# Kernel optimization log

Hardware: AMD Instinct MI355X
Metric: run time of the kernel (lower is better)

Reference implementation:

```python
import jax, jax.numpy as jnp
import numpy as np

# Config constants from the module
E = 64    # n_routed_experts
K = 6     # num_experts_per_tok
D = 128   # hidden_size
M = 80    # moe_intermediate_size
MS = 160  # shared expert intermediate = moe_intermediate_size * n_shared_experts
B, S = 64, 256

def _init_w(k, shape, fan_in):
    # kaiming_uniform(a=sqrt(5)) used by nn.Linear / MoEGate: bound = 1/sqrt(fan_in)
    bound = 1.0 / np.sqrt(fan_in)
    return jax.random.uniform(k, shape, jnp.float32, -bound, bound)

def setup_inputs() -> dict:
    key = jax.random.key(0)
    ks = jax.random.split(key, 8)
    return {
        "hidden_states": jax.random.normal(ks[0], (B, S, D), jnp.float32),
        "gate_w": _init_w(ks[1], (E, D), D),        # MoEGate.linear.weight [E, gating_dim]
        "wg": _init_w(ks[2], (E, D, M), D),          # stacked expert gate_proj (transposed)
        "wu": _init_w(ks[3], (E, D, M), D),          # stacked expert up_proj
        "wd": _init_w(ks[4], (E, M, D), M),          # stacked expert down_proj
        "swg": _init_w(ks[5], (D, MS), D),           # shared expert gate_proj
        "swu": _init_w(ks[6], (D, MS), D),           # shared expert up_proj
        "swd": _init_w(ks[7], (MS, D), MS),          # shared expert down_proj
    }

def reference(hidden_states, gate_w, wg, wu, wd, swg, swu, swd):
    orig_shape = hidden_states.shape
    x = hidden_states.reshape(-1, D)                       # [T, D] flat tokens
    T = x.shape[0]
    # --- MoEGate ('all_agent' mode): softmax scoring + top-k + renorm ---
    scores = jax.nn.softmax(x @ gate_w.T, axis=-1)          # [T, E]
    topk_w, topk_idx = jax.lax.top_k(scores, K)             # [T, K]
    topk_w = topk_w / (jnp.sum(topk_w, axis=-1, keepdims=True) + 1e-20)
    # Scatter top-k weights into dense per-expert combine weights [T, E]
    cw = jnp.zeros_like(scores).at[jnp.arange(T)[:, None], topk_idx].add(topk_w)
    # --- Routed experts: SiLU-gated MLP per expert, combined by cw ---
    g = jax.nn.silu(jnp.einsum('td,edm->tem', x, wg)) * jnp.einsum('td,edm->tem', x, wu)
    y = jnp.einsum('tem,emd,te->td', g, wd, cw)             # down-proj + weighted combine
    # --- Shared experts ---
    shared = (jax.nn.silu(x @ swg) * (x @ swu)) @ swd       # [T, D]
    return (y + shared).reshape(orig_shape)
```

## Files before the change

kernel.cpp:

```cpp
#include <hip/hip_runtime.h>
#include <hip/hip_bf16.h>
#include <math.h>


typedef unsigned short ushort_t;
typedef __attribute__((ext_vector_type(8))) short bf16x8;
typedef __attribute__((ext_vector_type(4))) float f32x4;

#define EALL  66

#define OFF_TOPKI 16384
#define OFF_WORK  409600
#define OFF_TOPKW 802816
#define OFF_PERM  1196032
#define OFF_PERMW 1589248
#define OFF_POS2  1982464
#define OFF_YPERM 2375680
#define OFF_YSH   27541504
#define OFF_WGT   31735808
#define OFF_WUT   33087488
#define OFF_WDP   34439168
#define OFF_XB    36061184
#define OFF_HIST  40255488
#define OFF_BOFF  40321024
#define NEED_FAST 40386560
#define FOFF_YBUF 2375680
#define FOFF_WGT  10764288
#define FOFF_WUT  12115968
#define FOFF_WDP  13467648
#define FOFF_XB   15089664
#define FOFF_HIST 19283968
#define FOFF_BOFF 19349504

__device__ __forceinline__ float bf2f(ushort_t u) {
    unsigned int x = ((unsigned int)u) << 16;
    float f; __builtin_memcpy(&f, &x, 4); return f;
}
__device__ __forceinline__ ushort_t f2bf(float f) {
    unsigned int x; __builtin_memcpy(&x, &f, 4);
    unsigned int r = (x + 0x7fffu + ((x >> 16) & 1u)) >> 16;
    return (ushort_t)r;
}
__device__ __forceinline__ float ldin(const void* p, int i, int f32m) {
    return f32m ? ((const float*)p)[i] : bf2f(((const ushort_t*)p)[i]);
}
__device__ __forceinline__ int detect_f32m(const ushort_t* gw) {
    int lane = threadIdx.x & 63;
    int cnt = 0;
    #pragma unroll
    for (int j = 0; j < 4; ++j) {
        ushort_t u = gw[lane * 4 + j];
        if (((u >> 7) & 0xFF) >= 0x7C) cnt++;
    }
    #pragma unroll
    for (int off = 32; off; off >>= 1) cnt += __shfl_xor(cnt, off);
    return (cnt >= 8) ? 1 : 0;
}
__device__ __forceinline__ void gl16(void* l, const void* g) {
    __builtin_amdgcn_global_load_lds(
        (const __attribute__((address_space(1))) void*)g,
        (__attribute__((address_space(3))) void*)l, 16, 0, 0);
}

__global__ __launch_bounds__(1024) void k_pg(const void* x, const void* gw,
        const void* wg, const void* wu, const void* wd,
        const void* swg, const void* swu, const void* swd,
        ushort_t* wgT, ushort_t* wuT, ushort_t* wdP,
        ushort_t* xB, int* topk_i, float* topk_w, int* histPart) {
    __shared__ __align__(16) char smem[41984];
    int tid = threadIdx.x, bid = blockIdx.x;
    int f32m = detect_f32m((const ushort_t*)gw);

    if (bid < 3 * EALL) {
        float* lds = (float*)smem;
        int mat = bid / EALL, e = bid % EALL;
        if (mat < 2) {
            const void* src  = (mat == 0) ? wg  : wu;
            const void* ssrc = (mat == 0) ? swg : swu;
            for (int i = tid; i < 10240; i += 1024) {
                int d = i / 80, m = i % 80;
                float v = (e < 64) ? ldin(src, e * 10240 + i, f32m)
                                   : ldin(ssrc, d * 160 + (e - 64) * 80 + m, f32m);
                lds[d * 81 + m] = v;
            }
            __syncthreads();
            ushort_t* dst = ((mat == 0) ? wgT : wuT) + e * 10240;
            for (int o = tid; o < 10240; o += 1024) {
                int m = o >> 7, d = o & 127;
                dst[o] = f2bf(lds[d * 81 + m]);
            }
        } else {
            for (int i = tid; i < 10240; i += 1024) {
                float v = (e < 64) ? ldin(wd, e * 10240 + i, f32m)
                                   : ldin(swd, (e - 64) * 10240 + i, f32m);
                int m = i >> 7, d = i & 127;
                lds[m * 129 + d] = v;
            }
            __syncthreads();
            ushort_t* dst = wdP + e * 12288;
            for (int o = tid; o < 12288; o += 1024) {
                int d = o / 96, m = o % 96;
                dst[o] = (m < 80) ? f2bf(lds[m * 129 + d]) : (ushort_t)0;
            }
        }
        return;
    }

    float* gwl  = (float*)smem;
    float (*xl)[128] = (float(*)[128])(smem + 33280);
    int*   histL = (int*)(smem + 41472);
    int b = bid - 3 * EALL;
    for (int i = tid; i < 8192; i += 1024)
        gwl[(i >> 7) * 130 + (i & 127)] = ldin(gw, i, f32m);
    if (tid < 64) histL[tid] = 0;
    __syncthreads();
    int wv = tid >> 6, lane = tid & 63;
    for (int q = 0; q < 4; ++q) {
        int t = b * 64 + wv * 4 + q;
        float xv0, xv1;
        if (f32m) {
            float2 v = ((const float2*)((const float*)x + t * 128))[lane];
            xv0 = v.x; xv1 = v.y;
        } else {
            unsigned int pr = *(const unsigned int*)((const ushort_t*)x + t * 128 + lane * 2);
            xv0 = bf2f((ushort_t)(pr & 0xffffu));
            xv1 = bf2f((ushort_t)(pr >> 16));
        }
        float2 xw; xw.x = xv0; xw.y = xv1;
        *(float2*)&xl[wv][lane * 2] = xw;
        unsigned int packed = (unsigned int)f2bf(xv0) | ((unsigned int)f2bf(xv1) << 16);
        *(unsigned int*)(xB + t * 128 + lane * 2) = packed;
        float acc = 0.f;
        #pragma unroll
        for (int d2 = 0; d2 < 64; ++d2) {
            float2 xv = *(const float2*)&xl[wv][d2 * 2];
            float2 gv = *(const float2*)&gwl[lane * 130 + d2 * 2];
            acc = fmaf(xv.x, gv.x, acc);
            acc = fmaf(xv.y, gv.y, acc);
        }
        float mx = acc;
        #pragma unroll
        for (int off = 32; off; off >>= 1) mx = fmaxf(mx, __shfl_xor(mx, off));
        float p = expf(acc - mx);
        float sm = p;
        #pragma unroll
        for (int off = 32; off; off >>= 1) sm += __shfl_xor(sm, off);
        float sc = p / sm;
        float cur = sc;
        float wk6[6]; int ik[6];
        #pragma unroll
        for (int k = 0; k < 6; ++k) {
            float bv = cur; int bi = lane;
            #pragma unroll
            for (int off = 1; off < 64; off <<= 1) {
                float ov = __shfl_xor(bv, off); int oi = __shfl_xor(bi, off);
                if (ov > bv || (ov == bv && oi < bi)) { bv = ov; bi = oi; }
            }
            wk6[k] = bv; ik[k] = bi;
            if (lane == bi) cur = -INFINITY;
        }
        if (lane == 0) {
            float den = wk6[0] + wk6[1] + wk6[2] + wk6[3] + wk6[4] + wk6[5] + 1e-20f;
            #pragma unroll
            for (int k = 0; k < 6; ++k) {
                topk_i[t * 6 + k] = ik[k];
                topk_w[t * 6 + k] = wk6[k] / den;
                atomicAdd(&histL[ik[k]], 1);
            }
        }
    }
    __syncthreads();
    if (tid < 64) histPart[tid * 256 + b] = histL[tid];
}

__global__ __launch_bounds__(256) void k_scatter(int* Wi, const int* histPart,
        const int* topk_i, const float* topk_w, int* perm, float* permw, int* pos2) {
    __shared__ int hl[16384];
    __shared__ int cntL[64], exclL[64], lcur[64];
    int tid = threadIdx.x, lane = tid & 63, wv = tid >> 6, b = blockIdx.x;
    for (int j = tid; j < 16384; j += 256) hl[j] = histPart[j];
    __syncthreads();
    for (int ei = 0; ei < 16; ++ei) {
        int e = wv * 16 + ei;
        int carry = 0;
        for (int r = 0; r < 4; ++r) {
            int v = hl[e * 256 + r * 64 + lane];
            int incl = v;
            #pragma unroll
            for (int off = 1; off < 64; off <<= 1) {
                int ts = __shfl_up(incl, off);
                if (lane >= off) incl += ts;
            }
            hl[e * 256 + r * 64 + lane] = carry + incl - v;
            carry += __shfl(incl, 63);
        }
        if (lane == 0) cntL[e] = carry;
    }
    __syncthreads();
    if (tid == 0) {
        int s = 0;
        for (int e = 0; e < 64; ++e) { exclL[e] = s; s += cntL[e]; }
    }
    __syncthreads();
    if (b == 0 && tid < 64) { Wi[tid] = cntL[tid]; Wi[64 + tid] = exclL[tid]; }
    if (tid < 64) lcur[tid] = hl[tid * 256 + b] + exclL[tid];
    __syncthreads();
    for (int i = tid; i < 384; i += 256) {
        int g = b * 384 + i;
        int e = topk_i[g];
        float w = topk_w[g];
        int p = atomicAdd(&lcur[e], 1);
        perm[p]  = b * 64 + i / 6;
        permw[p] = w;
        pos2[g]  = p;
    }
}

template<int FAST>
__global__ __launch_bounds__(256) void k_expert(const ushort_t* x, const ushort_t* wgT,
        const ushort_t* wuT, const ushort_t* wdP, const int* Wi,
        const int* perm, const float* permw, ushort_t* yperm, ushort_t* ysh, float* ybuf) {
    __shared__ __align__(16) char hl[32768];
    __shared__ __align__(16) char bufA[8192];
    __shared__ __align__(16) char bufB[8192];

    int tid = threadIdx.x, lid = tid & 63, wv = tid >> 6;
    int bid = blockIdx.x;
    int kg  = (lid >> 4) * 16;
    int kq8 = (lid >> 4) * 8;

    int e, c;
    if (bid < 256) {
        e = 64; c = bid;
    } else {
        int cnt_l = Wi[lid];
        int nc = (cnt_l + 127) >> 7;
        int incl = nc;
        #pragma unroll
        for (int off = 1; off < 64; off <<= 1) {
            int t2 = __shfl_up(incl, off);
            if (lid >= off) incl += t2;
        }
        int totalR = __shfl(incl, 63);
        int rb = bid - 256;
        if (rb >= totalR) return;
        int epref = incl - nc;
        unsigned long long m = __ballot(rb >= epref && rb < incl);
        int src = (int)__builtin_ctzll(m);
        e = src;
        c = rb - __shfl(epref, src);
    }

    if (e < 64) {
        int n = Wi[e], base = Wi[64 + e];
        int nrows = n - c * 128; if (nrows > 128) nrows = 128;

        bf16x8 a[2][4];
        #pragma unroll
        for (int tr = 0; tr < 2; ++tr) {
            int arow = wv * 32 + tr * 16 + (lid & 15);
            int r = (arow < nrows) ? arow : (nrows - 1);
            int t = perm[base + c * 128 + r];
            #pragma unroll
            for (int k = 0; k < 4; ++k)
                a[tr][k] = *(const bf16x8*)(x + t * 128 + k * 32 + kq8);
        }

        const ushort_t* gS = wgT + e * 10240;
        const ushort_t* uS = wuT + e * 10240;

        #pragma unroll
        for (int g = 0; g < 3; ++g) {
            int rbase = g * 32;
            int units = (g == 2) ? 256 : 512;
            #pragma unroll
            for (int i = 0; i < 2; ++i) {
                int s = i * 256 + tid;
                if (s < units) {
                    int row = rbase + (s >> 4);
                    int sc = (s & 15) ^ (row & 7);
                    gl16(bufA + (size_t)s * 16, gS + row * 128 + sc * 8);
                    gl16(bufB + (size_t)s * 16, uS + row * 128 + sc * 8);
                }
            }
            __syncthreads();
            int nmi = (g == 2) ? 1 : 2;
            for (int m2 = 0; m2 < nmi; ++m2) {
                int mi = 2 * g + m2;
                int brow = mi * 16 + (lid & 15);
                int lro = (brow - rbase) * 256;
                int bsw = (brow & 7) << 4;
                f32x4 ag[2], au[2];
                #pragma unroll
                for (int tr = 0; tr < 2; ++tr) {
                    ag[tr] = (f32x4){0.f, 0.f, 0.f, 0.f};
                    au[tr] = (f32x4){0.f, 0.f, 0.f, 0.f};
                }
                #pragma unroll
                for (int k = 0; k < 4; ++k) {
                    int bo = lro + (((k * 64) + kg) ^ bsw);
                    bf16x8 bg = *(const bf16x8*)(bufA + bo);
                    bf16x8 bu = *(const bf16x8*)(bufB + bo);
                    #pragma unroll
                    for (int tr = 0; tr < 2; ++tr) {
                        ag[tr] = __builtin_amdgcn_mfma_f32_16x16x32_bf16(a[tr][k], bg, ag[tr], 0, 0, 0);
                        au[tr] = __builtin_amdgcn_mfma_f32_16x16x32_bf16(a[tr][k], bu, au[tr], 0, 0, 0);
                    }
                }
                #pragma unroll
                for (int tr = 0; tr < 2; ++tr) {
                    #pragma unroll
                    for (int rg = 0; rg < 4; ++rg) {
                        float gg = ag[tr][rg], uu2 = au[tr][rg];
                        float h = (gg / (1.f + __expf(-gg))) * uu2;
                        int row = wv * 32 + tr * 16 + (lid >> 4) * 4 + rg;
                        int cb = (mi * 16 + (lid & 15)) * 2;
                        *(ushort_t*)(hl + row * 256 + (cb ^ ((row & 7) << 4))) = f2bf(h);
                    }
                }
            }
            __syncthreads();
        }

        {
            int r = wv * 32 + (lid >> 1), ch = 10 + (lid & 1);
            uint4 z = {0u, 0u, 0u, 0u};
            *(uint4*)(hl + r * 256 + ((ch * 16) ^ ((r & 7) << 4))) = z;
        }
        bf16x8 bfr[2][3];
        #pragma unroll
        for (int tf = 0; tf < 2; ++tf) {
            int brow = wv * 32 + tf * 16 + (lid & 15);
            #pragma unroll
            for (int k = 0; k < 3; ++k)
                bfr[tf][k] = *(const bf16x8*)(hl + brow * 256 + (((k * 64) + kg) ^ ((brow & 7) << 4)));
        }

        f32x4 acc[8][2];
        #pragma unroll
        for (int dt = 0; dt < 8; ++dt) {
            acc[dt][0] = (f32x4){0.f, 0.f, 0.f, 0.f};
            acc[dt][1] = (f32x4){0.f, 0.f, 0.f, 0.f};
        }
        const ushort_t* dS = wdP + e * 12288;
        #pragma unroll
        for (int h = 0; h < 2; ++h) {
            #pragma unroll
            for (int i = 0; i < 2; ++i) {
                int s = i * 256 + tid;
                int r = s >> 4, ch = s & 15;
                int rowA = h * 64 + r;
                int scA = ch ^ (rowA & 7);
                int offA = (scA < 12) ? scA * 8 : 0;
                gl16(bufA + (size_t)s * 16, dS + rowA * 96 + offA);
                int rowB = rowA + 32;
                int scB = ch ^ (rowB & 7);
                int offB = (scB < 12) ? scB * 8 : 0;
                gl16(bufB + (size_t)s * 16, dS + rowB * 96 + offB);
            }
            __syncthreads();
            #pragma unroll
            for (int d2 = 0; d2 < 4; ++d2) {
                int dt = h * 4 + d2;
                int grow = dt * 16 + (lid & 15);
                int lr = (d2 & 1) * 16 + (lid & 15);
                const char* wb = (d2 < 2) ? bufA : bufB;
                bf16x8 ad[3];
                #pragma unroll
                for (int k = 0; k < 3; ++k)
                    ad[k] = *(const bf16x8*)(wb + lr * 256 + (((k * 64) + kg) ^ ((grow & 7) << 4)));
                #pragma unroll
                for (int tf = 0; tf < 2; ++tf) {
                    f32x4 cc = acc[dt][tf];
                    #pragma unroll
                    for (int k = 0; k < 3; ++k)
                        cc = __builtin_amdgcn_mfma_f32_16x16x32_bf16(ad[k], bfr[tf][k], cc, 0, 0, 0);
                    acc[dt][tf] = cc;
                }
            }
            __syncthreads();
        }

        #pragma unroll
        for (int tf = 0; tf < 2; ++tf) {
            int rloc = wv * 32 + tf * 16 + (lid & 15);
            int rc = (rloc < nrows) ? rloc : (nrows - 1);
            float w = FAST ? permw[base + c * 128 + rc] : 0.f;
            #pragma unroll
            for (int dt = 0; dt < 8; ++dt) {
                if (FAST) {
                    int cb = (dt * 16 + (lid >> 4) * 4) * 2;
                    ushort_t o[4];
                    #pragma unroll
                    for (int rg = 0; rg < 4; ++rg) o[rg] = f2bf(acc[dt][tf][rg] * w);
                    *(uint2*)(hl + rloc * 256 + (cb ^ ((rloc & 7) << 4))) = *(const uint2*)o;
                } else {
                    if (rloc < nrows) {
                        int t = perm[base + c * 128 + rloc];
                        float w2 = permw[base + c * 128 + rloc];
                        int d0 = dt * 16 + (lid >> 4) * 4;
                        #pragma unroll
                        for (int rg = 0; rg < 4; ++rg)
                            atomicAdd(&ybuf[t * 128 + d0 + rg], acc[dt][tf][rg] * w2);
                    }
                }
            }
        }
        if (FAST) {
            #pragma unroll
            for (int ps = 0; ps < 8; ++ps) {
                int row = wv * 32 + ps * 4 + (lid >> 4);
                int cb = (lid & 15) * 16;
                uint4 v = *(const uint4*)(hl + row * 256 + (cb ^ ((row & 7) << 4)));
                if (row < nrows)
                    *(uint4*)(yperm + (size_t)(base + c * 128 + row) * 128 + (lid & 15) * 8) = v;
            }
        }
    } else {
        bf16x8 a1[4];
        int arow = wv * 16 + (lid & 15);
        int t0 = c * 64 + arow;
        #pragma unroll
        for (int k = 0; k < 4; ++k)
            a1[k] = *(const bf16x8*)(x + t0 * 128 + k * 32 + kq8);

        f32x4 acc[8];
        #pragma unroll
        for (int dt = 0; dt < 8; ++dt) acc[dt] = (f32x4){0.f, 0.f, 0.f, 0.f};

        for (int sub = 0; sub < 2; ++sub) {
            int ee = 64 + sub;
            const ushort_t* gS = wgT + ee * 10240;
            const ushort_t* uS = wuT + ee * 10240;

            #pragma unroll
            for (int g = 0; g < 3; ++g) {
                int rbase = g * 32;
                int units = (g == 2) ? 256 : 512;
                #pragma unroll
                for (int i = 0; i < 2; ++i) {
                    int s = i * 256 + tid;
                    if (s < units) {
                        int row = rbase + (s >> 4);
                        int sc = (s & 15) ^ (row & 7);
                        gl16(bufA + (size_t)s * 16, gS + row * 128 + sc * 8);
                        gl16(bufB + (size_t)s * 16, uS + row * 128 + sc * 8);
                    }
                }
                __syncthreads();
                int nmi = (g == 2) ? 1 : 2;
                for (int m2 = 0; m2 < nmi; ++m2) {
                    int mi = 2 * g + m2;
                    int brow = mi * 16 + (lid & 15);
                    int lro = (brow - rbase) * 256;
                    int bsw = (brow & 7) << 4;
                    f32x4 ag = {0.f, 0.f, 0.f, 0.f};
                    f32x4 au = {0.f, 0.f, 0.f, 0.f};
                    #pragma unroll
                    for (int k = 0; k < 4; ++k) {
                        int bo = lro + (((k * 64) + kg) ^ bsw);
                        bf16x8 bg = *(const bf16x8*)(bufA + bo);
                        bf16x8 bu = *(const bf16x8*)(bufB + bo);
                        ag = __builtin_amdgcn_mfma_f32_16x16x32_bf16(a1[k], bg, ag, 0, 0, 0);
                        au = __builtin_amdgcn_mfma_f32_16x16x32_bf16(a1[k], bu, au, 0, 0, 0);
                    }
                    #pragma unroll
                    for (int rg = 0; rg < 4; ++rg) {
                        float gg = ag[rg], uu2 = au[rg];
                        float h = (gg / (1.f + __expf(-gg))) * uu2;
                        int row = wv * 16 + (lid >> 4) * 4 + rg;
                        int cb = (mi * 16 + (lid & 15)) * 2;
                        *(ushort_t*)(hl + row * 256 + (cb ^ ((row & 7) << 4))) = f2bf(h);
                    }
                }
                __syncthreads();
            }
            if (sub == 0 && lid < 32) {
                int r = wv * 16 + (lid >> 1), ch = 10 + (lid & 1);
                uint4 z = {0u, 0u, 0u, 0u};
                *(uint4*)(hl + r * 256 + ((ch * 16) ^ ((r & 7) << 4))) = z;
            }
            bf16x8 bfr1[3];
            {
                int brow = wv * 16 + (lid & 15);
                #pragma unroll
                for (int k = 0; k < 3; ++k)
                    bfr1[k] = *(const bf16x8*)(hl + brow * 256 + (((k * 64) + kg) ^ ((brow & 7) << 4)));
            }

            const ushort_t* dS = wdP + ee * 12288;
            #pragma unroll
            for (int h = 0; h < 2; ++h) {
                #pragma unroll
                for (int i = 0; i < 2; ++i) {
                    int s = i * 256 + tid;
                    int r = s >> 4, ch = s & 15;
                    int rowA = h * 64 + r;
                    int scA = ch ^ (rowA & 7);
                    int offA = (scA < 12) ? scA * 8 : 0;
                    gl16(bufA + (size_t)s * 16, dS + rowA * 96 + offA);
                    int rowB = rowA + 32;
                    int scB = ch ^ (rowB & 7);
                    int offB = (scB < 12) ? scB * 8 : 0;
                    gl16(bufB + (size_t)s * 16, dS + rowB * 96 + offB);
                }
                __syncthreads();
                #pragma unroll
                for (int d2 = 0; d2 < 4; ++d2) {
                    int dt = h * 4 + d2;
                    int grow = dt * 16 + (lid & 15);
                    int lr = (d2 & 1) * 16 + (lid & 15);
                    const char* wb = (d2 < 2) ? bufA : bufB;
                    bf16x8 ad[3];
                    #pragma unroll
                    for (int k = 0; k < 3; ++k)
                        ad[k] = *(const bf16x8*)(wb + lr * 256 + (((k * 64) + kg) ^ ((grow & 7) << 4)));
                    f32x4 cc = acc[dt];
                    #pragma unroll
                    for (int k = 0; k < 3; ++k)
                        cc = __builtin_amdgcn_mfma_f32_16x16x32_bf16(ad[k], bfr1[k], cc, 0, 0, 0);
                    acc[dt] = cc;
                }
                __syncthreads();
            }
        }

        int rloc = wv * 16 + (lid & 15);
        if (FAST) {
            #pragma unroll
            for (int dt = 0; dt < 8; ++dt) {
                int cb = (dt * 16 + (lid >> 4) * 4) * 2;
                ushort_t o[4];
                #pragma unroll
                for (int rg = 0; rg < 4; ++rg) o[rg] = f2bf(acc[dt][rg]);
                *(uint2*)(hl + rloc * 256 + (cb ^ ((rloc & 7) << 4))) = *(const uint2*)o;
            }
            #pragma unroll
            for (int ps = 0; ps < 4; ++ps) {
                int row = wv * 16 + ps * 4 + (lid >> 4);
                int cb = (lid & 15) * 16;
                uint4 v = *(const uint4*)(hl + row * 256 + (cb ^ ((row & 7) << 4)));
                *(uint4*)(ysh + (size_t)(c * 64 + row) * 128 + (lid & 15) * 8) = v;
            }
        } else {
            int t = c * 64 + rloc;
            #pragma unroll
            for (int dt = 0; dt < 8; ++dt) {
                int d0 = dt * 16 + (lid >> 4) * 4;
                #pragma unroll
                for (int rg = 0; rg < 4; ++rg)
                    atomicAdd(&ybuf[t * 128 + d0 + rg], acc[dt][rg]);
            }
        }
    }
}

__global__ __launch_bounds__(256) void k_final_gather(const ushort_t* yperm,
        const ushort_t* ysh, const int* pos2, void* out, const ushort_t* gwDet) {
    int idx = blockIdx.x * 256 + threadIdx.x;
    int t = idx >> 4, cg = (idx & 15) * 8;
    int f32m = detect_f32m(gwDet);
    float acc[8];
    {
        uint4 v = *(const uint4*)(ysh + (size_t)t * 128 + cg);
        const ushort_t* u = (const ushort_t*)&v;
        #pragma unroll
        for (int j = 0; j < 8; ++j) acc[j] = bf2f(u[j]);
    }
    const int* pp = pos2 + t * 6;
    #pragma unroll
    for (int k = 0; k < 6; ++k) {
        int p = pp[k];
        uint4 v = *(const uint4*)(yperm + (size_t)p * 128 + cg);
        const ushort_t* u = (const ushort_t*)&v;
        #pragma unroll
        for (int j = 0; j < 8; ++j) acc[j] += bf2f(u[j]);
    }
    if (f32m) {
        float4 o0 = {acc[0], acc[1], acc[2], acc[3]};
        float4 o1 = {acc[4], acc[5], acc[6], acc[7]};
        float* op = (float*)out + (size_t)t * 128 + cg;
        *(float4*)op = o0; *(float4*)(op + 4) = o1;
    } else {
        ushort_t o[8];
        #pragma unroll
        for (int j = 0; j < 8; ++j) o[j] = f2bf(acc[j]);
        *(uint4*)((ushort_t*)out + (size_t)t * 128 + cg) = *(const uint4*)o;
    }
}

__global__ __launch_bounds__(256) void k_final_ybuf(const float* ybuf, void* out,
        const ushort_t* gwDet) {
    int i = blockIdx.x * 256 + threadIdx.x;
    int f32m = detect_f32m(gwDet);
    float4 v = ((const float4*)ybuf)[i];
    if (f32m) {
        ((float4*)out)[i] = v;
    } else {
        ushort4 o;
        o.x = f2bf(v.x); o.y = f2bf(v.y); o.z = f2bf(v.z); o.w = f2bf(v.w);
        ((ushort4*)out)[i] = o;
    }
}

extern "C" void kernel_launch(void* const* d_in, const int* in_sizes, int n_in,
                              void* d_out, int out_size, void* d_ws, size_t ws_size,
                              hipStream_t stream) {
    (void)in_sizes; (void)n_in; (void)out_size;
    const void* x   = d_in[0];
    const void* gw  = d_in[1];
    const void* wg  = d_in[2];
    const void* wu  = d_in[3];
    const void* wd  = d_in[4];
    const void* swg = d_in[5];
    const void* swu = d_in[6];
    const void* swd = d_in[7];

    char* ws = (char*)d_ws;
    int fast = (ws_size >= (size_t)NEED_FAST) ? 1 : 0;

    int*      Wi     = (int*)d_ws;
    int*      topk_i = (int*)(ws + OFF_TOPKI);
    float*    topk_w = (float*)(ws + OFF_TOPKW);
    int*      perm   = (int*)(ws + OFF_PERM);
    float*    permw  = (float*)(ws + OFF_PERMW);
    int*      pos2   = (int*)(ws + OFF_POS2);

    ushort_t* yperm = (ushort_t*)(ws + OFF_YPERM);
    ushort_t* ysh   = (ushort_t*)(ws + OFF_YSH);
    float*    ybuf  = (float*)(ws + FOFF_YBUF);
    ushort_t* wgT   = (ushort_t*)(ws + (fast ? OFF_WGT  : FOFF_WGT));
    ushort_t* wuT   = (ushort_t*)(ws + (fast ? OFF_WUT  : FOFF_WUT));
    ushort_t* wdP   = (ushort_t*)(ws + (fast ? OFF_WDP  : FOFF_WDP));
    ushort_t* xB    = (ushort_t*)(ws + (fast ? OFF_XB   : FOFF_XB));
    int*      histP = (int*)(ws + (fast ? OFF_HIST : FOFF_HIST));

    if (!fast) hipMemsetAsync(ybuf, 0, 16384 * 128 * 4, stream);

    k_pg<<<3 * EALL + 256, 1024, 0, stream>>>(x, gw, wg, wu, wd, swg, swu, swd,
                                              wgT, wuT, wdP, xB, topk_i, topk_w, histP);
    k_scatter<<<256, 256, 0, stream>>>(Wi, histP, topk_i, topk_w, perm, permw, pos2);
    if (fast) {
        k_expert<1><<<1088, 256, 0, stream>>>(xB, wgT, wuT, wdP, Wi, perm, permw, yperm, ysh, ybuf);
        k_final_gather<<<1024, 256, 0, stream>>>(yperm, ysh, pos2, d_out, (const ushort_t*)gw);
    } else {
        k_expert<0><<<1088, 256, 0, stream>>>(xB, wgT, wuT, wdP, Wi, perm, permw, yperm, ysh, ybuf);
        k_final_ybuf<<<2048, 256, 0, stream>>>(ybuf, d_out, (const ushort_t*)gw);
    }
}
```

Baseline: 93.53 us.

## Prefetch expert gate/up and down weights into larger LDS buffers upfront

Enlarges the LDS weight staging buffers so that most of the gate/up weights and the whole down-projection matrix are loaded asynchronously at the start of each expert block. The global-to-LDS transfers then overlap with the token gather and the gate/up MFMA work. This cuts the number of load/sync rounds from five to two per expert. The down-projection matrix gets a new 192-byte row layout with a split swizzle, which avoids the padded 256-byte rows and the dummy loads. LDS use per block rises to about 80KB, which may lower occupancy.

```diff
diff --git a/kernel.cpp b/kernel.cpp
--- a/kernel.cpp
+++ b/kernel.cpp
@@ -10,7 +10,6 @@
 #define EALL  66
 
 #define OFF_TOPKI 16384
-#define OFF_WORK  409600
 #define OFF_TOPKW 802816
 #define OFF_PERM  1196032
 #define OFF_PERMW 1589248
@@ -61,6 +60,9 @@
         (const __attribute__((address_space(1))) void*)g,
         (__attribute__((address_space(3))) void*)l, 16, 0, 0);
 }
+__device__ __forceinline__ int dswz(int ch, int r) {
+    return (ch < 8) ? (ch ^ (r & 7)) : (8 + ((ch - 8) ^ (r & 3)));
+}
 
 __global__ __launch_bounds__(1024) void k_pg(const void* x, const void* gw,
         const void* wg, const void* wu, const void* wd,
@@ -221,8 +223,8 @@
         const ushort_t* wuT, const ushort_t* wdP, const int* Wi,
         const int* perm, const float* permw, ushort_t* yperm, ushort_t* ysh, float* ybuf) {
     __shared__ __align__(16) char hl[32768];
-    __shared__ __align__(16) char bufA[8192];
-    __shared__ __align__(16) char bufB[8192];
+    __shared__ __align__(16) char bufW[24576];
+    __shared__ __align__(16) char bufD[24576];
 
     int tid = threadIdx.x, lid = tid & 63, wv = tid >> 6;
     int bid = blockIdx.x;
@@ -255,6 +257,26 @@
         int n = Wi[e], base = Wi[64 + e];
         int nrows = n - c * 128; if (nrows > 128) nrows = 128;
 
+        const ushort_t* gS = wgT + e * 10240;
+        const ushort_t* uS = wuT + e * 10240;
+        const ushort_t* dS = wdP + e * 12288;
+
+        #pragma unroll
+        for (int i = 0; i < 3; ++i) {
+            int u = i * 256 + tid;
+            int r = u >> 4, ch = u & 15;
+            int cc = ch ^ (r & 7);
+            gl16(bufW + (size_t)u * 16, gS + r * 128 + cc * 8);
+            gl16(bufW + 12288 + (size_t)u * 16, uS + r * 128 + cc * 8);
+        }
+        #pragma unroll
+        for (int i = 0; i < 6; ++i) {
+            int u = i * 256 + tid;
+            int r = u / 12, d = u % 12;
+            int cc = dswz(d, r);
+            gl16(bufD + (size_t)u * 16, dS + r * 96 + cc * 8);
+        }
+
         bf16x8 a[2][4];
         #pragma unroll
         for (int tr = 0; tr < 2; ++tr) {
@@ -265,61 +287,86 @@
             for (int k = 0; k < 4; ++k)
                 a[tr][k] = *(const bf16x8*)(x + t * 128 + k * 32 + kq8);
         }
-
-        const ushort_t* gS = wgT + e * 10240;
-        const ushort_t* uS = wuT + e * 10240;
-
-        #pragma unroll
-        for (int g = 0; g < 3; ++g) {
-            int rbase = g * 32;
-            int units = (g == 2) ? 256 : 512;
-            #pragma unroll
-            for (int i = 0; i < 2; ++i) {
-                int s = i * 256 + tid;
-                if (s < units) {
-                    int row = rbase + (s >> 4);
-                    int sc = (s & 15) ^ (row & 7);
-                    gl16(bufA + (size_t)s * 16, gS + row * 128 + sc * 8);
-                    gl16(bufB + (size_t)s * 16, uS + row * 128 + sc * 8);
-                }
-            }
-            __syncthreads();
-            int nmi = (g == 2) ? 1 : 2;
-            for (int m2 = 0; m2 < nmi; ++m2) {
-                int mi = 2 * g + m2;
-                int brow = mi * 16 + (lid & 15);
-                int lro = (brow - rbase) * 256;
-                int bsw = (brow & 7) << 4;
-                f32x4 ag[2], au[2];
+        __syncthreads();
+
+        #pragma unroll
+        for (int mi = 0; mi < 3; ++mi) {
+            int brow = mi * 16 + (lid & 15);
+            int bro = brow * 256, bsw = (brow & 7) << 4;
+            f32x4 ag[2], au[2];
+            #pragma unroll
+            for (int tr = 0; tr < 2; ++tr) {
+                ag[tr] = (f32x4){0.f, 0.f, 0.f, 0.f};
+                au[tr] = (f32x4){0.f, 0.f, 0.f, 0.f};
+            }
+            #pragma unroll
+            for (int k = 0; k < 4; ++k) {
+                int bo = bro + (((k * 64) + kg) ^ bsw);
+                bf16x8 bg = *(const bf16x8*)(bufW + bo);
+                bf16x8 bu = *(const bf16x8*)(bufW + 12288 + bo);
                 #pragma unroll
                 for (int tr = 0; tr < 2; ++tr) {
-                    ag[tr] = (f32x4){0.f, 0.f, 0.f, 0.f};
-                    au[tr] = (f32x4){0.f, 0.f, 0.f, 0.f};
-                }
-                #pragma unroll
-                for (int k = 0; k < 4; ++k) {
-                    int bo = lro + (((k * 64) + kg) ^ bsw);
-                    bf16x8 bg = *(const bf16x8*)(bufA + bo);
-                    bf16x8 bu = *(const bf16x8*)(bufB + bo);
-                    #pragma unroll
-                    for (int tr = 0; tr < 2; ++tr) {
-                        ag[tr] = __builtin_amdgcn_mfma_f32_16x16x32_bf16(a[tr][k], bg, ag[tr], 0, 0, 0);
-                        au[tr] = __builtin_amdgcn_mfma_f32_16x16x32_bf16(a[tr][k], bu, au[tr], 0, 0, 0);
-                    }
-                }
+                    ag[tr] = __builtin_amdgcn_mfma_f32_16x16x32_bf16(a[tr][k], bg, ag[tr], 0, 0, 0);
+                    au[tr] = __builtin_amdgcn_mfma_f32_16x16x32_bf16(a[tr][k], bu, au[tr], 0, 0, 0);
+                }
+            }
+            #pragma unroll
+            for (int tr = 0; tr < 2; ++tr) {
+                #pragma unroll
+                for (int rg = 0; rg < 4; ++rg) {
+                    float g = ag[tr][rg], uu2 = au[tr][rg];
+                    float h = (g / (1.f + __expf(-g))) * uu2;
+                    int row = wv * 32 + tr * 16 + (lid >> 4) * 4 + rg;
+                    int cb = (mi * 16 + (lid & 15)) * 2;
+                    *(ushort_t*)(hl + row * 256 + (cb ^ ((row & 7) << 4))) = f2bf(h);
+                }
+            }
+        }
+        __syncthreads();
+
+        #pragma unroll
+        for (int i = 0; i < 2; ++i) {
+            int u = i * 256 + tid;
+            int lr = u >> 4, ch = u & 15;
+            int gr = 48 + lr;
+            int cc = ch ^ (lr & 7);
+            gl16(bufW + (size_t)u * 16, gS + gr * 128 + cc * 8);
+            gl16(bufW + 12288 + (size_t)u * 16, uS + gr * 128 + cc * 8);
+        }
+        __syncthreads();
+
+        #pragma unroll
+        for (int mi = 3; mi < 5; ++mi) {
+            int brow = mi * 16 + (lid & 15);
+            int bro = (brow - 48) * 256, bsw = (brow & 7) << 4;
+            f32x4 ag[2], au[2];
+            #pragma unroll
+            for (int tr = 0; tr < 2; ++tr) {
+                ag[tr] = (f32x4){0.f, 0.f, 0.f, 0.f};
+                au[tr] = (f32x4){0.f, 0.f, 0.f, 0.f};
+            }
+            #pragma unroll
+            for (int k = 0; k < 4; ++k) {
+                int bo = bro + (((k * 64) + kg) ^ bsw);
+                bf16x8 bg = *(const bf16x8*)(bufW + bo);
+                bf16x8 bu = *(const bf16x8*)(bufW + 12288 + bo);
                 #pragma unroll
                 for (int tr = 0; tr < 2; ++tr) {
-                    #pragma unroll
-                    for (int rg = 0; rg < 4; ++rg) {
-                        float gg = ag[tr][rg], uu2 = au[tr][rg];
-                        float h = (gg / (1.f + __expf(-gg))) * uu2;
-                        int row = wv * 32 + tr * 16 + (lid >> 4) * 4 + rg;
-                        int cb = (mi * 16 + (lid & 15)) * 2;
-                        *(ushort_t*)(hl + row * 256 + (cb ^ ((row & 7) << 4))) = f2bf(h);
-                    }
-                }
-            }
-            __syncthreads();
+                    ag[tr] = __builtin_amdgcn_mfma_f32_16x16x32_bf16(a[tr][k], bg, ag[tr], 0, 0, 0);
+                    au[tr] = __builtin_amdgcn_mfma_f32_16x16x32_bf16(a[tr][k], bu, au[tr], 0, 0, 0);
+                }
+            }
+            #pragma unroll
+            for (int tr = 0; tr < 2; ++tr) {
+                #pragma unroll
+                for (int rg = 0; rg < 4; ++rg) {
+                    float g = ag[tr][rg], uu2 = au[tr][rg];
+                    float h = (g / (1.f + __expf(-g))) * uu2;
+                    int row = wv * 32 + tr * 16 + (lid >> 4) * 4 + rg;
+                    int cb = (mi * 16 + (lid & 15)) * 2;
+                    *(ushort_t*)(hl + row * 256 + (cb ^ ((row & 7) << 4))) = f2bf(h);
+                }
+            }
         }
 
         {
@@ -342,43 +389,24 @@
             acc[dt][0] = (f32x4){0.f, 0.f, 0.f, 0.f};
             acc[dt][1] = (f32x4){0.f, 0.f, 0.f, 0.f};
         }
-        const ushort_t* dS = wdP + e * 12288;
-        #pragma unroll
-        for (int h = 0; h < 2; ++h) {
-            #pragma unroll
-            for (int i = 0; i < 2; ++i) {
-                int s = i * 256 + tid;
-                int r = s >> 4, ch = s & 15;
-                int rowA = h * 64 + r;
-                int scA = ch ^ (rowA & 7);
-                int offA = (scA < 12) ? scA * 8 : 0;
-                gl16(bufA + (size_t)s * 16, dS + rowA * 96 + offA);
-                int rowB = rowA + 32;
-                int scB = ch ^ (rowB & 7);
-                int offB = (scB < 12) ? scB * 8 : 0;
-                gl16(bufB + (size_t)s * 16, dS + rowB * 96 + offB);
-            }
-            __syncthreads();
-            #pragma unroll
-            for (int d2 = 0; d2 < 4; ++d2) {
-                int dt = h * 4 + d2;
-                int grow = dt * 16 + (lid & 15);
-                int lr = (d2 & 1) * 16 + (lid & 15);
-                const char* wb = (d2 < 2) ? bufA : bufB;
-                bf16x8 ad[3];
+        #pragma unroll
+        for (int dt = 0; dt < 8; ++dt) {
+            int grow = dt * 16 + (lid & 15);
+            bf16x8 ad[3];
+            #pragma unroll
+            for (int k = 0; k < 3; ++k) {
+                int c0 = k * 4 + (lid >> 4);
+                int ph = dswz(c0, grow);
+                ad[k] = *(const bf16x8*)(bufD + grow * 192 + ph * 16);
+            }
+            #pragma unroll
+            for (int tf = 0; tf < 2; ++tf) {
+                f32x4 cc = acc[dt][tf];
                 #pragma unroll
                 for (int k = 0; k < 3; ++k)
-                    ad[k] = *(const bf16x8*)(wb + lr * 256 + (((k * 64) + kg) ^ ((grow & 7) << 4)));
-                #pragma unroll
-                for (int tf = 0; tf < 2; ++tf) {
-                    f32x4 cc = acc[dt][tf];
-                    #pragma unroll
-                    for (int k = 0; k < 3; ++k)
-                        cc = __builtin_amdgcn_mfma_f32_16x16x32_bf16(ad[k], bfr[tf][k], cc, 0, 0, 0);
-                    acc[dt][tf] = cc;
-                }
-            }
-            __syncthreads();
+                    cc = __builtin_amdgcn_mfma_f32_16x16x32_bf16(ad[k], bfr[tf][k], cc, 0, 0, 0);
+                acc[dt][tf] = cc;
+            }
         }
 
         #pragma unroll
@@ -432,48 +460,83 @@
             int ee = 64 + sub;
             const ushort_t* gS = wgT + ee * 10240;
             const ushort_t* uS = wuT + ee * 10240;
-
-            #pragma unroll
-            for (int g = 0; g < 3; ++g) {
-                int rbase = g * 32;
-                int units = (g == 2) ? 256 : 512;
-                #pragma unroll
-                for (int i = 0; i < 2; ++i) {
-                    int s = i * 256 + tid;
-                    if (s < units) {
-                        int row = rbase + (s >> 4);
-                        int sc = (s & 15) ^ (row & 7);
-                        gl16(bufA + (size_t)s * 16, gS + row * 128 + sc * 8);
-                        gl16(bufB + (size_t)s * 16, uS + row * 128 + sc * 8);
-                    }
-                }
-                __syncthreads();
-                int nmi = (g == 2) ? 1 : 2;
-                for (int m2 = 0; m2 < nmi; ++m2) {
-                    int mi = 2 * g + m2;
-                    int brow = mi * 16 + (lid & 15);
-                    int lro = (brow - rbase) * 256;
-                    int bsw = (brow & 7) << 4;
-                    f32x4 ag = {0.f, 0.f, 0.f, 0.f};
-                    f32x4 au = {0.f, 0.f, 0.f, 0.f};
-                    #pragma unroll
-                    for (int k = 0; k < 4; ++k) {
-                        int bo = lro + (((k * 64) + kg) ^ bsw);
-                        bf16x8 bg = *(const bf16x8*)(bufA + bo);
-                        bf16x8 bu = *(const bf16x8*)(bufB + bo);
-                        ag = __builtin_amdgcn_mfma_f32_16x16x32_bf16(a1[k], bg, ag, 0, 0, 0);
-                        au = __builtin_amdgcn_mfma_f32_16x16x32_bf16(a1[k], bu, au, 0, 0, 0);
-                    }
-                    #pragma unroll
-                    for (int rg = 0; rg < 4; ++rg) {
-                        float gg = ag[rg], uu2 = au[rg];
-                        float h = (gg / (1.f + __expf(-gg))) * uu2;
-                        int row = wv * 16 + (lid >> 4) * 4 + rg;
-                        int cb = (mi * 16 + (lid & 15)) * 2;
-                        *(ushort_t*)(hl + row * 256 + (cb ^ ((row & 7) << 4))) = f2bf(h);
-                    }
-                }
-                __syncthreads();
+            const ushort_t* dS = wdP + ee * 12288;
+
+            #pragma unroll
+            for (int i = 0; i < 3; ++i) {
+                int u = i * 256 + tid;
+                int r = u >> 4, ch = u & 15;
+                int cc = ch ^ (r & 7);
+                gl16(bufW + (size_t)u * 16, gS + r * 128 + cc * 8);
+                gl16(bufW + 12288 + (size_t)u * 16, uS + r * 128 + cc * 8);
+            }
+            #pragma unroll
+            for (int i = 0; i < 6; ++i) {
+                int u = i * 256 + tid;
+                int r = u / 12, d = u % 12;
+                int cc = dswz(d, r);
+                gl16(bufD + (size_t)u * 16, dS + r * 96 + cc * 8);
+            }
+            __syncthreads();
+
+            #pragma unroll
+            for (int mi = 0; mi < 3; ++mi) {
+                int brow = mi * 16 + (lid & 15);
+                int bro = brow * 256, bsw = (brow & 7) << 4;
+                f32x4 ag = {0.f, 0.f, 0.f, 0.f};
+                f32x4 au = {0.f, 0.f, 0.f, 0.f};
+                #pragma unroll
+                for (int k = 0; k < 4; ++k) {
+                    int bo = bro + (((k * 64) + kg) ^ bsw);
+                    bf16x8 bg = *(const bf16x8*)(bufW + bo);
+                    bf16x8 bu = *(const bf16x8*)(bufW + 12288 + bo);
+                    ag = __builtin_amdgcn_mfma_f32_16x16x32_bf16(a1[k], bg, ag, 0, 0, 0);
+                    au = __builtin_amdgcn_mfma_f32_16x16x32_bf16(a1[k], bu, au, 0, 0, 0);
+                }
+                #pragma unroll
+                for (int rg = 0; rg < 4; ++rg) {
+                    float g = ag[rg], uu2 = au[rg];
+                    float h = (g / (1.f + __expf(-g))) * uu2;
+                    int row = wv * 16 + (lid >> 4) * 4 + rg;
+                    int cb = (mi * 16 + (lid & 15)) * 2;
+                    *(ushort_t*)(hl + row * 256 + (cb ^ ((row & 7) << 4))) = f2bf(h);
+                }
+            }
+            __syncthreads();
+
+            #pragma unroll
+            for (int i = 0; i < 2; ++i) {
+                int u = i * 256 + tid;
+                int lr = u >> 4, ch = u & 15;
+                int gr = 48 + lr;
+                int cc = ch ^ (lr & 7);
+                gl16(bufW + (size_t)u * 16, gS + gr * 128 + cc * 8);
+                gl16(bufW + 12288 + (size_t)u * 16, uS + gr * 128 + cc * 8);
+            }
+            __syncthreads();
+
+            #pragma unroll
+            for (int mi = 3; mi < 5; ++mi) {
+                int brow = mi * 16 + (lid & 15);
+                int bro = (brow - 48) * 256, bsw = (brow & 7) << 4;
+                f32x4 ag = {0.f, 0.f, 0.f, 0.f};
+                f32x4 au = {0.f, 0.f, 0.f, 0.f};
+                #pragma unroll
+                for (int k = 0; k < 4; ++k) {
+                    int bo = bro + (((k * 64) + kg) ^ bsw);
+                    bf16x8 bg = *(const bf16x8*)(bufW + bo);
+                    bf16x8 bu = *(const bf16x8*)(bufW + 12288 + bo);
+                    ag = __builtin_amdgcn_mfma_f32_16x16x32_bf16(a1[k], bg, ag, 0, 0, 0);
+                    au = __builtin_amdgcn_mfma_f32_16x16x32_bf16(a1[k], bu, au, 0, 0, 0);
+                }
+                #pragma unroll
+                for (int rg = 0; rg < 4; ++rg) {
+                    float g = ag[rg], uu2 = au[rg];
+                    float h = (g / (1.f + __expf(-g))) * uu2;
+                    int row = wv * 16 + (lid >> 4) * 4 + rg;
+                    int cb = (mi * 16 + (lid & 15)) * 2;
+                    *(ushort_t*)(hl + row * 256 + (cb ^ ((row & 7) << 4))) = f2bf(h);
+                }
             }
             if (sub == 0 && lid < 32) {
                 int r = wv * 16 + (lid >> 1), ch = 10 + (lid & 1);
@@ -488,41 +551,23 @@
                     bfr1[k] = *(const bf16x8*)(hl + brow * 256 + (((k * 64) + kg) ^ ((brow & 7) << 4)));
             }
 
-            const ushort_t* dS = wdP + ee * 12288;
-            #pragma unroll
-            for (int h = 0; h < 2; ++h) {
-                #pragma unroll
-                for (int i = 0; i < 2; ++i) {
-                    int s = i * 256 + tid;
-                    int r = s >> 4, ch = s & 15;
-                    int rowA = h * 64 + r;
-                    int scA = ch ^ (rowA & 7);
-                    int offA = (scA < 12) ? scA * 8 : 0;
-                    gl16(bufA + (size_t)s * 16, dS + rowA * 96 + offA);
-                    int rowB = rowA + 32;
-                    int scB = ch ^ (rowB & 7);
-                    int offB = (scB < 12) ? scB * 8 : 0;
-                    gl16(bufB + (size_t)s * 16, dS + rowB * 96 + offB);
-                }
-                __syncthreads();
-                #pragma unroll
-                for (int d2 = 0; d2 < 4; ++d2) {
-                    int dt = h * 4 + d2;
-                    int grow = dt * 16 + (lid & 15);
-                    int lr = (d2 & 1) * 16 + (lid & 15);
-                    const char* wb = (d2 < 2) ? bufA : bufB;
-                    bf16x8 ad[3];
-                    #pragma unroll
-                    for (int k = 0; k < 3; ++k)
-                        ad[k] = *(const bf16x8*)(wb + lr * 256 + (((k * 64) + kg) ^ ((grow & 7) << 4)));
-                    f32x4 cc = acc[dt];
-                    #pragma unroll
-                    for (int k = 0; k < 3; ++k)
-                        cc = __builtin_amdgcn_mfma_f32_16x16x32_bf16(ad[k], bfr1[k], cc, 0, 0, 0);
-                    acc[dt] = cc;
-                }
-                __syncthreads();
-            }
+            #pragma unroll
+            for (int dt = 0; dt < 8; ++dt) {
+                int grow = dt * 16 + (lid & 15);
+                bf16x8 ad[3];
+                #pragma unroll
+                for (int k = 0; k < 3; ++k) {
+                    int c0 = k * 4 + (lid >> 4);
+                    int ph = dswz(c0, grow);
+                    ad[k] = *(const bf16x8*)(bufD + grow * 192 + ph * 16);
+                }
+                f32x4 cc = acc[dt];
+                #pragma unroll
+                for (int k = 0; k < 3; ++k)
+                    cc = __builtin_amdgcn_mfma_f32_16x16x32_bf16(ad[k], bfr1[k], cc, 0, 0, 0);
+                acc[dt] = cc;
+            }
+            if (sub == 0) __syncthreads();
         }
 
         int rloc = wv * 16 + (lid & 15);
```

Result: slower. 103.2 us (+10.3%).
